# Kernel tuning notes

Measured on AMD Instinct MI355X. Metric: run time of the kernel, lower is better.

## Reference

```python
import jax, jax.numpy as jnp
import numpy as np

ROUTE_NUM = 3
EPS = 1e-8


def squash(s):
    # s: [bs, J, d2]; squash along last dim
    sq = jnp.sum(s * s, axis=-1, keepdims=True)
    return (sq / (1.0 + sq)) * s / jnp.sqrt(sq + EPS)


def setup_inputs() -> dict:
    key = jax.random.key(0)
    k1, k2, k3 = jax.random.split(key, 3)
    bs, in_dim, s1 = 64, 256, 16
    out_dim, J = 32, 64           # J = num_out_caps (as_final_output)
    I = s1 * s1                   # num_in_caps = 256
    x = jax.random.normal(k1, (bs, in_dim, s1, s1), dtype=jnp.float32)
    b_init = jax.random.uniform(k2, (bs, J, I), dtype=jnp.float32)
    W = jax.random.normal(k3, (out_dim * J, in_dim), dtype=jnp.float32) * 0.05
    Wb = jnp.zeros((out_dim * J,), dtype=jnp.float32)
    return {"x": x, "b_init": b_init, "W": W, "Wb": Wb}


def reference(x, b_init, W, Wb):
    bs = x.shape[0]
    J, I = b_init.shape[1], b_init.shape[2]
    d2 = W.shape[0] // J
    # 1x1 conv == per-pixel GEMM: [bs, OUT, s1, s1]
    pred = jnp.einsum('oi,bihw->bohw', W, x) + Wb[None, :, None, None]
    # [bs, J, d2, I] -> [bs, I, J, d2]
    pred = pred.reshape(bs, J, d2, I).transpose(0, 3, 1, 2)
    b = b_init
    v = None
    for _ in range(ROUTE_NUM):
        c = jax.nn.softmax(b, axis=1)                  # softmax over out-caps J
        s = jnp.einsum('bji,bijd->bjd', c, pred)       # weighted sum over in-caps
        v = squash(s)                                  # [bs, J, d2]
        db = jax.lax.stop_gradient(jnp.einsum('bjd,bijd->bji', v, pred))
        b = b + db
    return v
```

## Files before the change

kernel.cpp:

```cpp
#include <hip/hip_runtime.h>
#include <hip/hip_bf16.h>

#define BS    64
#define KDIM  256
#define ICAP  256
#define JCAP  64
#define D2    32
#define OUTD  2048
#define NPART 16

typedef short bf16x8 __attribute__((ext_vector_type(8)));
typedef float f32x4  __attribute__((ext_vector_type(4)));

static __device__ __forceinline__ float bf2f(unsigned u16) {
  union { unsigned u; float f; } v; v.u = u16 << 16; return v.f;
}
static __device__ __forceinline__ unsigned short f2bf(float x) {
  union { float f; unsigned u; } v; v.f = x;
  unsigned r = v.u + 0x7fffu + ((v.u >> 16) & 1u);
  return (unsigned short)(r >> 16);
}
static __device__ __forceinline__ void unpack8(uint4 u, float* f) {
  f[0] = bf2f(u.x & 0xffffu); f[1] = bf2f(u.x >> 16);
  f[2] = bf2f(u.y & 0xffffu); f[3] = bf2f(u.y >> 16);
  f[4] = bf2f(u.z & 0xffffu); f[5] = bf2f(u.z >> 16);
  f[6] = bf2f(u.w & 0xffffu); f[7] = bf2f(u.w >> 16);
}
static __device__ __forceinline__ void gl_lds16(const unsigned short* g,
                                                unsigned short* l) {
  __builtin_amdgcn_global_load_lds(
      (const __attribute__((address_space(1))) unsigned int*)g,
      (__attribute__((address_space(3))) unsigned int*)l, 16, 0, 0);
}

__global__ __launch_bounds__(256) void prep(
    const float* __restrict__ W, const float* __restrict__ x,
    const float* __restrict__ Binit,
    unsigned short* __restrict__ Wbf, unsigned short* __restrict__ xT,
    unsigned short* __restrict__ c0)
{
  __shared__ union {
    float Ls[64][65];
    float Bs[64][68];
  } sm;
  const int t   = threadIdx.x;
  const int blk = blockIdx.x;

  if (blk < 256) {
    const int g = blk * 256 + t;
    const float* s = W + (size_t)g * 8;
    f32x4 a = *(const f32x4*)s;
    f32x4 b = *(const f32x4*)(s + 4);
    uint4 o;
    o.x = (unsigned)f2bf(a.x) | ((unsigned)f2bf(a.y) << 16);
    o.y = (unsigned)f2bf(a.z) | ((unsigned)f2bf(a.w) << 16);
    o.z = (unsigned)f2bf(b.x) | ((unsigned)f2bf(b.y) << 16);
    o.w = (unsigned)f2bf(b.z) | ((unsigned)f2bf(b.w) << 16);
    *(uint4*)(Wbf + (size_t)g * 8) = o;
  } else if (blk < 1280) {
    const int bid = blk - 256;
    const int i0  = (bid & 3) * 64;
    const int k0  = ((bid >> 2) & 3) * 64;
    const int b   = bid >> 4;
    for (int it = 0; it < 4; ++it) {
      const int k  = it * 16 + (t >> 4);
      const int i4 = (t & 15) * 4;
      f32x4 v = *(const f32x4*)(x + ((size_t)(b * KDIM + k0 + k) * ICAP) + i0 + i4);
      sm.Ls[k][i4 + 0] = v.x; sm.Ls[k][i4 + 1] = v.y;
      sm.Ls[k][i4 + 2] = v.z; sm.Ls[k][i4 + 3] = v.w;
    }
    __syncthreads();
    const int i  = t >> 2;
    const int kc = (t & 3) * 16;
    unsigned pk[8];
    for (int q = 0; q < 8; ++q) {
      float lo = sm.Ls[kc + 2 * q][i];
      float hi = sm.Ls[kc + 2 * q + 1][i];
      pk[q] = (unsigned)f2bf(lo) | ((unsigned)f2bf(hi) << 16);
    }
    unsigned short* dst = xT + ((size_t)(b * ICAP + i0 + i) * KDIM) + k0 + kc;
    uint4 s0; s0.x = pk[0]; s0.y = pk[1]; s0.z = pk[2]; s0.w = pk[3];
    uint4 s1; s1.x = pk[4]; s1.y = pk[5]; s1.z = pk[6]; s1.w = pk[7];
    *(uint4*)dst       = s0;
    *(uint4*)(dst + 8) = s1;
  } else {
    const int bid = blk - 1280;
    const int b   = bid >> 2;
    const int q   = bid & 3;
    {
      const int j  = t >> 2;
      const int c4 = (t & 3) * 16;
      const float* src = Binit + ((size_t)(b * JCAP + j) * ICAP) + q * 64 + c4;
      for (int r = 0; r < 4; ++r) {
        f32x4 v = *(const f32x4*)(src + r * 4);
        *(f32x4*)&sm.Bs[j][c4 + r * 4] = v;
      }
    }
    __syncthreads();
    if (t < 64) {
      const int ii = t;
      float m = -3.0e38f;
      for (int j = 0; j < 64; ++j) m = fmaxf(m, sm.Bs[j][ii]);
      float se = 0.f;
      for (int j = 0; j < 64; ++j) se += __expf(sm.Bs[j][ii] - m);
      const float inv = 1.0f / se;
      unsigned short* dst = c0 + ((size_t)(b * ICAP + q * 64 + ii) * JCAP);
      for (int qq = 0; qq < 8; ++qq) {
        unsigned pk[4];
        for (int h = 0; h < 4; ++h) {
          float lo = __expf(sm.Bs[qq * 8 + 2 * h][ii] - m) * inv;
          float hi = __expf(sm.Bs[qq * 8 + 2 * h + 1][ii] - m) * inv;
          pk[h] = (unsigned)f2bf(lo) | ((unsigned)f2bf(hi) << 16);
        }
        uint4 s; s.x = pk[0]; s.y = pk[1]; s.z = pk[2]; s.w = pk[3];
        *(uint4*)(dst + qq * 8) = s;
      }
    }
  }
}

__global__ __launch_bounds__(256) void gemm_pred(
    const unsigned short* __restrict__ Wbf,
    const unsigned short* __restrict__ xT,
    const float* __restrict__ Wb,
    const unsigned short* __restrict__ c0,
    unsigned short* __restrict__ P,
    float* __restrict__ s0part)
{
  __shared__ union {
    unsigned short AB[2][128][64];
    struct {
      unsigned short C[64][136];
      unsigned short c0t[128][4];
    } ep;
  } sm;

  const int tid = threadIdx.x;
  const int b   = blockIdx.z;
  const int o0  = blockIdx.x * 128;
  const int i0  = blockIdx.y * 128;
  const int l   = tid & 63;
  const int m   = l & 15;
  const int w   = tid >> 6;
  const int wo  = (w & 1) * 64;

  const int srow = l >> 3;
  const int gch  = (l & 7) ^ srow;

  f32x4 acc[4][4];
  for (int a = 0; a < 4; ++a)
    for (int c = 0; c < 4; ++c) acc[a][c] = (f32x4){0.f, 0.f, 0.f, 0.f};

  for (int r = 0; r < 4; ++r) {
    const int k0 = r * 64;
    __syncthreads();
    for (int c = 0; c < 4; ++c) {
      const int q   = w * 4 + c;
      const int row = q * 8 + srow;
      gl_lds16(Wbf + (size_t)(o0 + row) * KDIM + k0 + gch * 8,
               &sm.AB[0][q * 8][0]);
      gl_lds16(xT + ((size_t)(b * ICAP + i0 + row) * KDIM) + k0 + gch * 8,
               &sm.AB[1][q * 8][0]);
    }
    __syncthreads();
    for (int ks = 0; ks < 2; ++ks) {
      const int clog = ks * 4 + (l >> 4);
      bf16x8 af[4], bfg[4];
      for (int ti = 0; ti < 4; ++ti) {
        const int row = wo + 16 * ti + m;
        af[ti] = *(const bf16x8*)&sm.AB[0][row][(clog ^ (m & 7)) * 8];
      }
      for (int tj = 0; tj < 4; ++tj) {
        const int row = (w >> 1) * 64 + 16 * tj + m;
        bfg[tj] = *(const bf16x8*)&sm.AB[1][row][(clog ^ (m & 7)) * 8];
      }
      for (int ti = 0; ti < 4; ++ti)
        for (int tj = 0; tj < 4; ++tj)
          acc[ti][tj] = __builtin_amdgcn_mfma_f32_16x16x32_bf16(
              af[ti], bfg[tj], acc[ti][tj], 0, 0, 0);
    }
  }

  __syncthreads();
  if (tid < 128) {
    const int j0 = blockIdx.x * 4;
    uint2 v = *(const uint2*)(c0 + ((size_t)(b * ICAP + i0 + tid) * JCAP) + j0);
    *(uint2*)&sm.ep.c0t[tid][0] = v;
  }

  for (int half = 0; half < 2; ++half) {
    __syncthreads();
    if ((w >> 1) == half) {
      const int q4 = (l >> 4) * 4;
      for (int ti = 0; ti < 4; ++ti) {
        const int ob = wo + 16 * ti + q4;
        f32x4 wb4 = *(const f32x4*)(Wb + o0 + ob);
        for (int tj = 0; tj < 4; ++tj) {
          const int ii = 16 * tj + m;
          f32x4 a = acc[ti][tj];
          uint2 pk;
          pk.x = (unsigned)f2bf(a.x + wb4.x) | ((unsigned)f2bf(a.y + wb4.y) << 16);
          pk.y = (unsigned)f2bf(a.z + wb4.z) | ((unsigned)f2bf(a.w + wb4.w) << 16);
          *(uint2*)&sm.ep.C[ii][ob] = pk;
        }
      }
    }
    __syncthreads();
    for (int rr = 0; rr < 4; ++rr) {
      const int id  = rr * 256 + tid;
      const int row = id >> 4;
      const int seg = id & 15;
      uint4 v = *(const uint4*)&sm.ep.C[row][seg * 8];
      *(uint4*)(P + ((size_t)(b * ICAP + i0 + half * 64 + row) * OUTD) + o0 + seg * 8) = v;
    }
    {
      const int oc = tid & 127;
      const int q  = tid >> 7;
      const int jj = oc >> 5;
      float s = 0.f;
      for (int r2 = 0; r2 < 32; ++r2) {
        const int il = q * 32 + r2;
        s += bf2f(sm.ep.C[il][oc]) * bf2f(sm.ep.c0t[half * 64 + il][jj]);
      }
      const int p = blockIdx.y * 4 + half * 2 + q;
      s0part[((size_t)(b * 8 + p) * OUTD) + o0 + oc] = s;
    }
  }
}

__global__ __launch_bounds__(256) void squash_v(
    const float* __restrict__ part,
    const int npart,
    float* __restrict__ dst)
{
  const int tid = threadIdx.x;
  const int b   = blockIdx.x;
  const float* base = part + (size_t)b * npart * OUTD + tid * 8;
  float s[8] = {0.f,0.f,0.f,0.f,0.f,0.f,0.f,0.f};
  for (int p = 0; p < npart; ++p) {
    f32x4 a = *(const f32x4*)(base + (size_t)p * OUTD);
    f32x4 c = *(const f32x4*)(base + (size_t)p * OUTD + 4);
    s[0] += a.x; s[1] += a.y; s[2] += a.z; s[3] += a.w;
    s[4] += c.x; s[5] += c.y; s[6] += c.z; s[7] += c.w;
  }
  float sq = 0.f;
  for (int c = 0; c < 8; ++c) sq += s[c] * s[c];
  sq += __shfl_xor(sq, 1, 64);
  sq += __shfl_xor(sq, 2, 64);
  float scale = (sq / (1.0f + sq)) / sqrtf(sq + 1e-8f);
  float* d = dst + (size_t)b * OUTD + tid * 8;
  f32x4 t0 = {scale*s[0], scale*s[1], scale*s[2], scale*s[3]};
  f32x4 t1 = {scale*s[4], scale*s[5], scale*s[6], scale*s[7]};
  *(f32x4*)d       = t0;
  *(f32x4*)(d + 4) = t1;
}

__global__ __launch_bounds__(256) void route_fused(
    const unsigned short* __restrict__ P,
    const float* __restrict__ Binit,
    float* __restrict__ B1,
    const float* __restrict__ Vin,
    float* __restrict__ part_out,
    const int pass)
{
  __shared__ float Ps[4][2112];

  const int tid = threadIdx.x;
  const int l   = tid & 63;
  const int w   = tid >> 6;
  const int b   = blockIdx.x >> 4;
  const int g   = blockIdx.x & 15;

  float vv[32];
  {
    const float* vp = Vin + (size_t)b * OUTD + l * D2;
    for (int q = 0; q < 8; ++q) {
      f32x4 t = *(const f32x4*)(vp + q * 4);
      vv[q*4+0] = t.x; vv[q*4+1] = t.y; vv[q*4+2] = t.z; vv[q*4+3] = t.w;
    }
  }

  const int i0 = g * 16 + w * 4;
  float bold[4];
  if (pass == 1) {
    f32x4 t = *(const f32x4*)(Binit + (size_t)(b * JCAP + l) * ICAP + i0);
    bold[0] = t.x; bold[1] = t.y; bold[2] = t.z; bold[3] = t.w;
  } else {
    for (int ii = 0; ii < 4; ++ii)
      bold[ii] = B1[((size_t)(b * ICAP + i0 + ii)) * JCAP + l];
  }

  float sacc[32];
  for (int k = 0; k < 32; ++k) sacc[k] = 0.f;

  const unsigned short* pbase = P + ((size_t)(b * ICAP + i0) * OUTD) + l * D2;
  uint4 ubuf[2][4];
  for (int q = 0; q < 4; ++q) ubuf[0][q] = *(const uint4*)(pbase + q * 8);
  for (int q = 0; q < 4; ++q) ubuf[1][q] = *(const uint4*)(pbase + OUTD + q * 8);

#pragma unroll
  for (int ii = 0; ii < 4; ++ii) {
    uint4 cur[4];
    for (int q = 0; q < 4; ++q) cur[q] = ubuf[ii & 1][q];
    if (ii + 2 < 4)
      for (int q = 0; q < 4; ++q)
        ubuf[ii & 1][q] = *(const uint4*)(pbase + (size_t)(ii + 2) * OUTD + q * 8);

    float db = 0.f;
    for (int q = 0; q < 4; ++q) {
      float ps[8]; unpack8(cur[q], ps);
      for (int k = 0; k < 8; ++k) db += ps[k] * vv[q * 8 + k];
    }
    float bnew = bold[ii] + db;
    if (pass == 1) B1[((size_t)(b * ICAP + i0 + ii)) * JCAP + l] = bnew;

    float mx = bnew;
    for (int off = 1; off < 64; off <<= 1) mx = fmaxf(mx, __shfl_xor(mx, off, 64));
    float e = __expf(bnew - mx);
    float se = e;
    for (int off = 1; off < 64; off <<= 1) se += __shfl_xor(se, off, 64);
    float c = e / se;
    for (int q = 0; q < 4; ++q) {
      float ps[8]; unpack8(cur[q], ps);
      for (int k = 0; k < 8; ++k) sacc[q * 8 + k] += c * ps[k];
    }
  }

  for (int k = 0; k < 32; ++k) Ps[w][l * 33 + k] = sacc[k];
  __syncthreads();

  {
    const int o0 = tid * 8;
    float s[8];
    for (int c = 0; c < 8; ++c) {
      const int o = o0 + c, j = o >> 5, d = o & 31, idx = j * 33 + d;
      s[c] = Ps[0][idx] + Ps[1][idx] + Ps[2][idx] + Ps[3][idx];
    }
    float* dst = part_out + ((size_t)(b * NPART + g)) * OUTD + o0;
    f32x4 t0 = {s[0], s[1], s[2], s[3]};
    f32x4 t1 = {s[4], s[5], s[6], s[7]};
    *(f32x4*)dst       = t0;
    *(f32x4*)(dst + 4) = t1;
  }
}

extern "C" void kernel_launch(void* const* d_in, const int* in_sizes, int n_in,
                              void* d_out, int out_size, void* d_ws, size_t ws_size,
                              hipStream_t stream) {
  const float* x  = (const float*)d_in[0];
  const float* bi = (const float*)d_in[1];
  const float* W  = (const float*)d_in[2];
  const float* Wb = (const float*)d_in[3];
  float* out = (float*)d_out;

  char* ws = (char*)d_ws;
  const size_t MiB = 1024 * 1024;
  unsigned short* P        = (unsigned short*)ws;
  unsigned short* xT       = (unsigned short*)(ws + 64 * MiB);
  float*          partial1 = (float*)(ws + 64 * MiB);
  float*          s0part   = (float*)(ws + 72 * MiB);
  unsigned short* Wbf      = (unsigned short*)(ws + 76 * MiB);
  unsigned short* c0       = (unsigned short*)(ws + 77 * MiB);
  float*          partial2 = (float*)(ws + 72 * MiB);
  float* B1                = (float*)(ws + 80 * MiB);
  float* V1                = (float*)(ws + 84 * MiB);
  float* V2                = (float*)(ws + 84 * MiB + 512 * 1024);

  prep<<<dim3(1536), 256, 0, stream>>>(W, x, bi, Wbf, xT, c0);
  gemm_pred<<<dim3(16, 2, 64), 256, 0, stream>>>(Wbf, xT, Wb, c0, P, s0part);
  squash_v<<<dim3(64), 256, 0, stream>>>(s0part, 8, V1);
  route_fused<<<dim3(1024), 256, 0, stream>>>(P, bi, B1, V1, partial1, 1);
  squash_v<<<dim3(64), 256, 0, stream>>>(partial1, NPART, V2);
  route_fused<<<dim3(1024), 256, 0, stream>>>(P, bi, B1, V2, partial2, 2);
  squash_v<<<dim3(64), 256, 0, stream>>>(partial2, NPART, out);
}
```

Baseline: 162.6 us.

## Fuse squash into routing kernel and recompute logits from summed V

Each route_fused block now sums the partial s vectors and applies squash itself, which removes two separate squash_v launches. Instead of storing and reloading the intermediate logits B1, the second pass uses linearity of db in v: it routes with V1+V2 against the original b_init. This removes the B1 write and the strided B1 read, at the cost of every block redundantly reducing partials and squashing.

```diff
diff --git a/kernel.cpp b/kernel.cpp
--- a/kernel.cpp
+++ b/kernel.cpp
@@ -258,12 +258,16 @@
 __global__ __launch_bounds__(256) void route_fused(
     const unsigned short* __restrict__ P,
     const float* __restrict__ Binit,
-    float* __restrict__ B1,
-    const float* __restrict__ Vin,
-    float* __restrict__ part_out,
-    const int pass)
+    const float* __restrict__ part_in,
+    const int npart_in,
+    const float* __restrict__ Vprev,
+    float* __restrict__ Vout,
+    float* __restrict__ part_out)
 {
-  __shared__ float Ps[4][2112];
+  __shared__ union {
+    float Vs[2112];
+    float Ps[4][2112];
+  } sm;
 
   const int tid = threadIdx.x;
   const int l   = tid & 63;
@@ -271,23 +275,49 @@
   const int b   = blockIdx.x >> 4;
   const int g   = blockIdx.x & 15;
 
+  {
+    const float* base = part_in + (size_t)b * npart_in * OUTD + tid * 8;
+    float s[8] = {0.f,0.f,0.f,0.f,0.f,0.f,0.f,0.f};
+    for (int p = 0; p < npart_in; ++p) {
+      f32x4 a = *(const f32x4*)(base + (size_t)p * OUTD);
+      f32x4 c = *(const f32x4*)(base + (size_t)p * OUTD + 4);
+      s[0] += a.x; s[1] += a.y; s[2] += a.z; s[3] += a.w;
+      s[4] += c.x; s[5] += c.y; s[6] += c.z; s[7] += c.w;
+    }
+    float sq = 0.f;
+    for (int c = 0; c < 8; ++c) sq += s[c] * s[c];
+    sq += __shfl_xor(sq, 1, 64);
+    sq += __shfl_xor(sq, 2, 64);
+    float scale = (sq / (1.0f + sq)) / sqrtf(sq + 1e-8f);
+    const int j  = tid >> 2;
+    const int d0 = (tid & 3) * 8;
+    float vloc[8];
+    for (int c = 0; c < 8; ++c) vloc[c] = scale * s[c];
+    if (Vout && g == 0) {
+      float* vd = Vout + (size_t)b * OUTD + tid * 8;
+      f32x4 t0 = {vloc[0], vloc[1], vloc[2], vloc[3]};
+      f32x4 t1 = {vloc[4], vloc[5], vloc[6], vloc[7]};
+      *(f32x4*)vd       = t0;
+      *(f32x4*)(vd + 4) = t1;
+    }
+    if (Vprev) {
+      const float* vp = Vprev + (size_t)b * OUTD + tid * 8;
+      f32x4 t0 = *(const f32x4*)vp;
+      f32x4 t1 = *(const f32x4*)(vp + 4);
+      vloc[0] += t0.x; vloc[1] += t0.y; vloc[2] += t0.z; vloc[3] += t0.w;
+      vloc[4] += t1.x; vloc[5] += t1.y; vloc[6] += t1.z; vloc[7] += t1.w;
+    }
+    for (int c = 0; c < 8; ++c) sm.Vs[j * 33 + d0 + c] = vloc[c];
+  }
+  __syncthreads();
   float vv[32];
-  {
-    const float* vp = Vin + (size_t)b * OUTD + l * D2;
-    for (int q = 0; q < 8; ++q) {
-      f32x4 t = *(const f32x4*)(vp + q * 4);
-      vv[q*4+0] = t.x; vv[q*4+1] = t.y; vv[q*4+2] = t.z; vv[q*4+3] = t.w;
-    }
-  }
+  for (int k = 0; k < 32; ++k) vv[k] = sm.Vs[l * 33 + k];
 
   const int i0 = g * 16 + w * 4;
   float bold[4];
-  if (pass == 1) {
+  {
     f32x4 t = *(const f32x4*)(Binit + (size_t)(b * JCAP + l) * ICAP + i0);
     bold[0] = t.x; bold[1] = t.y; bold[2] = t.z; bold[3] = t.w;
-  } else {
-    for (int ii = 0; ii < 4; ++ii)
-      bold[ii] = B1[((size_t)(b * ICAP + i0 + ii)) * JCAP + l];
   }
 
   float sacc[32];
@@ -312,7 +342,6 @@
       for (int k = 0; k < 8; ++k) db += ps[k] * vv[q * 8 + k];
     }
     float bnew = bold[ii] + db;
-    if (pass == 1) B1[((size_t)(b * ICAP + i0 + ii)) * JCAP + l] = bnew;
 
     float mx = bnew;
     for (int off = 1; off < 64; off <<= 1) mx = fmaxf(mx, __shfl_xor(mx, off, 64));
@@ -326,7 +355,8 @@
     }
   }
 
-  for (int k = 0; k < 32; ++k) Ps[w][l * 33 + k] = sacc[k];
+  __syncthreads();
+  for (int k = 0; k < 32; ++k) sm.Ps[w][l * 33 + k] = sacc[k];
   __syncthreads();
 
   {
@@ -334,7 +364,7 @@
     float s[8];
     for (int c = 0; c < 8; ++c) {
       const int o = o0 + c, j = o >> 5, d = o & 31, idx = j * 33 + d;
-      s[c] = Ps[0][idx] + Ps[1][idx] + Ps[2][idx] + Ps[3][idx];
+      s[c] = sm.Ps[0][idx] + sm.Ps[1][idx] + sm.Ps[2][idx] + sm.Ps[3][idx];
     }
     float* dst = part_out + ((size_t)(b * NPART + g)) * OUTD + o0;
     f32x4 t0 = {s[0], s[1], s[2], s[3]};
@@ -362,15 +392,11 @@
   unsigned short* Wbf      = (unsigned short*)(ws + 76 * MiB);
   unsigned short* c0       = (unsigned short*)(ws + 77 * MiB);
   float*          partial2 = (float*)(ws + 72 * MiB);
-  float* B1                = (float*)(ws + 80 * MiB);
-  float* V1                = (float*)(ws + 84 * MiB);
-  float* V2                = (float*)(ws + 84 * MiB + 512 * 1024);
+  float* V1                = (float*)(ws + 80 * MiB);
 
   prep<<<dim3(1536), 256, 0, stream>>>(W, x, bi, Wbf, xT, c0);
   gemm_pred<<<dim3(16, 2, 64), 256, 0, stream>>>(Wbf, xT, Wb, c0, P, s0part);
-  squash_v<<<dim3(64), 256, 0, stream>>>(s0part, 8, V1);
-  route_fused<<<dim3(1024), 256, 0, stream>>>(P, bi, B1, V1, partial1, 1);
-  squash_v<<<dim3(64), 256, 0, stream>>>(partial1, NPART, V2);
-  route_fused<<<dim3(1024), 256, 0, stream>>>(P, bi, B1, V2, partial2, 2);
+  route_fused<<<dim3(1024), 256, 0, stream>>>(P, bi, s0part, 8, nullptr, V1, partial1);
+  route_fused<<<dim3(1024), 256, 0, stream>>>(P, bi, partial1, NPART, V1, nullptr, partial2);
   squash_v<<<dim3(64), 256, 0, stream>>>(partial2, NPART, out);
 }
```

Result: no change. 164.8 us (+1.4%).
